# Kernel optimization log

Hardware: AMD Instinct MI355X
Metric: run time of the kernel (lower is better)

Reference implementation:

```python
import jax, jax.numpy as jnp
import numpy as np

L, BATCH, STATE_DIM, HIDDEN, ACTION_DIM = 2048, 32, 256, 1024, 64


def setup_inputs() -> dict:
    key = jax.random.key(0)
    k1, k2, k3, k4 = jax.random.split(key, 4)
    states = jax.random.normal(k1, (L, BATCH, STATE_DIM), dtype=jnp.float32)
    actions = jax.random.normal(k2, (L, BATCH, ACTION_DIM), dtype=jnp.float32)
    # Parameters, matching torch init: A_log = log(0.99), B/C weights ~ N(0, 0.01)
    A_log = jnp.full((HIDDEN,), np.log(0.99), dtype=jnp.float32)
    B_w = 0.01 * jax.random.normal(k3, (HIDDEN, STATE_DIM), dtype=jnp.float32)
    B_b = jnp.zeros((HIDDEN,), dtype=jnp.float32)
    C_w = 0.01 * jax.random.normal(k4, (ACTION_DIM, HIDDEN), dtype=jnp.float32)
    C_b = jnp.zeros((ACTION_DIM,), dtype=jnp.float32)
    log_std = jnp.zeros((ACTION_DIM,), dtype=jnp.float32)
    return {"states": states, "actions": actions, "A_log": A_log,
            "B_w": B_w, "B_b": B_b, "C_w": C_w, "C_b": C_b, "log_std": log_std}


def reference(states, actions, A_log, B_w, B_b, C_w, C_b, log_std):
    # b_t = B(states_t)  -> [L, batch, hidden]
    b = jnp.einsum('lbd,hd->lbh', states, B_w) + B_b
    # log_P[t] = cumsum over seq of broadcast A_log = (t+1) * A_log
    seq = states.shape[0]
    t = jnp.arange(1, seq + 1, dtype=states.dtype)  # [L]
    log_P = t[:, None, None] * A_log[None, None, :]  # [L, 1, hidden]
    P = jnp.exp(log_P)
    # h_t = P_t * cumsum_t(b_t / P_t)  (log-domain linear SSM scan)
    h = P * jnp.cumsum(b / P, axis=0)
    h = jnp.tanh(h)
    mus = jnp.einsum('lbh,ah->lba', h, C_w) + C_b  # [L, batch, action]
    std = jnp.exp(log_std)
    log_pi = (-0.5 * (jnp.log(jnp.asarray(2.0 * np.pi, dtype=mus.dtype)) + 2.0 * log_std)
              - 0.5 * ((actions - mus) / std) ** 2)
    return log_pi.sum(axis=-1)  # [L, batch]; torch squeeze(-1) is a no-op for batch>1
```

## Files before the change

kernel.cpp:

```cpp
#include <hip/hip_runtime.h>
#include <hip/hip_bf16.h>

typedef __attribute__((ext_vector_type(4))) float f32x4;
typedef __attribute__((ext_vector_type(8))) short bf16x8;

#define SDIM 256
#define HID 1024
#define ADIM 64
#define CHUNK 16
#define NCHUNK 128
#define NCH 32768

#define WS8_STB  67108864ull
#define WS8_SCB  100663296ull
#define WS8_BWB  117440512ull
#define WS8_CWB  117964800ull
#define WS8_NEED 118095872ull
#define WS_STB2  134217728ull
#define WS_SBUF2 134217728ull
#define WS_CBUF2 150994944ull
#define WS_BWB2  167772160ull
#define WS_CWB2  168296448ull
#define WS_NEED2 168427520ull

__device__ __forceinline__ unsigned short f2bf(float f) {
  unsigned int u = __float_as_uint(f);
  u += 0x7FFF + ((u >> 16) & 1);
  return (unsigned short)(u >> 16);
}
__device__ __forceinline__ float bf2f(unsigned short h) {
  return __uint_as_float(((unsigned int)h) << 16);
}
__device__ __forceinline__ float fast_exp2(float x) {
  float r;
  asm("v_exp_f32 %0, %1" : "=v"(r) : "v"(x));
  return r;
}
__device__ __forceinline__ float fast_rcp(float x) {
  float r;
  asm("v_rcp_f32 %0, %1" : "=v"(r) : "v"(x));
  return r;
}
#define LOG2E 1.4426950408889634f

#define GLDS16(gp, lp)                                                        \
  __builtin_amdgcn_global_load_lds(                                           \
      (const __attribute__((address_space(1))) unsigned int*)(gp),            \
      (__attribute__((address_space(3))) unsigned int*)(lp), 16, 0, 0)

#define CVT_SN 16777216
#define CVT_BN 262144
#define CVT_CN 65536
__global__ __launch_bounds__(256) void k_cvt(
    const float* __restrict__ s, const float* __restrict__ bw,
    const float* __restrict__ cw, unsigned short* __restrict__ sb,
    unsigned short* __restrict__ bwb, unsigned short* __restrict__ cwb,
    int perm) {
  long long f = ((long long)blockIdx.x * 256 + threadIdx.x) * 8;
  const float* src;
  unsigned short* dst;
  long long idx, didx;
  if (f < CVT_SN) {
    src = s; dst = sb; idx = f;
    if (perm) {
      long long m = f >> 8, col = f & 255;
      didx = ((m & 31) * 2048 + (m >> 5)) * 256 + col;
    } else didx = f;
  } else if (f < CVT_SN + CVT_BN) {
    src = bw; dst = bwb; idx = f - CVT_SN; didx = idx;
  } else {
    src = cw; dst = cwb; idx = f - CVT_SN - CVT_BN; didx = idx;
  }
  float4 a = *reinterpret_cast<const float4*>(src + idx);
  float4 b = *reinterpret_cast<const float4*>(src + idx + 4);
  ushort4 lo, hi;
  lo.x = f2bf(a.x); lo.y = f2bf(a.y); lo.z = f2bf(a.z); lo.w = f2bf(a.w);
  hi.x = f2bf(b.x); hi.y = f2bf(b.y); hi.z = f2bf(b.z); hi.w = f2bf(b.w);
  *reinterpret_cast<ushort4*>(dst + didx) = lo;
  *reinterpret_cast<ushort4*>(dst + didx + 4) = hi;
}

__device__ __forceinline__ void g1_compute(
    const char* bA, const char* bB, f32x4 (&acc)[4][4],
    int wm, int wn, int l15, int g) {
  bf16x8 af[4][2], bfv[4][2];
#pragma unroll
  for (int kk = 0; kk < 2; ++kk) {
    int slotsw = ((kk * 4 + g) ^ (l15 & 7)) * 16;
#pragma unroll
    for (int f = 0; f < 4; ++f) {
      af[f][kk] = *reinterpret_cast<const bf16x8*>(bA + (wm + f * 16 + l15) * 128 + slotsw);
      bfv[f][kk] = *reinterpret_cast<const bf16x8*>(bB + (wn + f * 16 + l15) * 128 + slotsw);
    }
  }
#pragma unroll
  for (int kk = 0; kk < 2; ++kk)
#pragma unroll
    for (int i = 0; i < 4; ++i)
#pragma unroll
      for (int j = 0; j < 4; ++j)
        acc[i][j] = __builtin_amdgcn_mfma_f32_16x16x32_bf16(
            bfv[j][kk], af[i][kk], acc[i][j], 0, 0, 0);
}

#define STAGE1(tile, buf)                                                     \
  {                                                                           \
    const int k0b_ = (tile) * 128;                                            \
    char* dA_ = lds + (buf) * 32768;                                          \
    char* dB_ = lds + 16384 + (buf) * 32768;                                  \
    _Pragma("unroll")                                                         \
    for (int p = 0; p < 4; ++p) {                                             \
      int chunk = wave * 4 + p;                                               \
      GLDS16((const char*)sb + ((size_t)(m0 + chunk * 8 + srow) * SDIM) * 2 + \
                 k0b_ + swslot * 16,                                          \
             dA_ + chunk * 1024);                                             \
      GLDS16((const char*)bwb + ((size_t)(n0 + chunk * 8 + srow) * SDIM) * 2 +\
                 k0b_ + swslot * 16,                                          \
             dB_ + chunk * 1024);                                             \
    }                                                                         \
  }

#define G1_PIPELINE()                                                         \
  STAGE1(0, 0);                                                               \
  for (int t = 0; t < 3; ++t) {                                               \
    const int cur = t & 1;                                                    \
    STAGE1(t + 1, cur ^ 1);                                                   \
    asm volatile("s_waitcnt vmcnt(8)" ::: "memory");                          \
    __builtin_amdgcn_s_barrier();                                             \
    __builtin_amdgcn_sched_barrier(0);                                        \
    g1_compute(lds + cur * 32768, lds + 16384 + cur * 32768, acc, wm, wn,     \
               l15, g);                                                       \
    __builtin_amdgcn_s_barrier();                                             \
    __builtin_amdgcn_sched_barrier(0);                                        \
  }                                                                           \
  asm volatile("s_waitcnt vmcnt(0)" ::: "memory");                            \
  __builtin_amdgcn_s_barrier();                                               \
  __builtin_amdgcn_sched_barrier(0);                                          \
  g1_compute(lds + 32768, lds + 16384 + 32768, acc, wm, wn, l15, g);          \
  __builtin_amdgcn_s_barrier();                                               \
  __builtin_amdgcn_sched_barrier(0);

__global__ __launch_bounds__(256) void k_gemm1p_f(
    const unsigned short* __restrict__ sb, const unsigned short* __restrict__ bwb,
    const float* __restrict__ Bb, const float* __restrict__ A_log,
    unsigned char* __restrict__ bout8, float* __restrict__ Sb) {
  __shared__ char lds[65536];
  const int tid = threadIdx.x;
  const int wave = tid >> 6, lane = tid & 63;
  const int l15 = lane & 15, g = lane >> 4;
  const int bx = blockIdx.x;
  const int swzb = (bx & 7) * 512 + (bx >> 3);
  const int mt = swzb >> 3, nt = swzb & 7;
  const int m0 = mt * 128, n0 = nt * 128;
  const int bb2 = mt >> 4;
  const int c0t = (mt & 15) * 8;
  const int wm = (wave >> 1) * 64, wn = (wave & 1) * 64;
  const int srow = lane >> 3;
  const int swslot = (lane & 7) ^ srow;

  f32x4 acc[4][4];
#pragma unroll
  for (int i = 0; i < 4; i++)
#pragma unroll
    for (int j = 0; j < 4; j++) acc[i][j] = (f32x4){0.f, 0.f, 0.f, 0.f};

  G1_PIPELINE();

  char* wb = lds + wave * 9216;
#pragma unroll
  for (int j = 0; j < 4; ++j) {
    float4 bb = *reinterpret_cast<const float4*>(Bb + n0 + wn + j * 16 + g * 4);
#pragma unroll
    for (int i = 0; i < 4; ++i) {
      ushort4 w;
      w.x = f2bf(acc[i][j][0] + bb.x);
      w.y = f2bf(acc[i][j][1] + bb.y);
      w.z = f2bf(acc[i][j][2] + bb.z);
      w.w = f2bf(acc[i][j][3] + bb.w);
      *reinterpret_cast<ushort4*>(wb + (i * 16 + l15) * 144 + j * 32 + g * 8) = w;
    }
  }
  const int h8 = lane & 7;
  const int lr = lane >> 3;
#pragma unroll
  for (int tt = 0; tt < 8; ++tt) {
    int ml = lr + tt * 8;
    int4 v = *reinterpret_cast<const int4*>(wb + ml * 144 + h8 * 16);
    unsigned int u[4] = {(unsigned)v.x, (unsigned)v.y, (unsigned)v.z,
                         (unsigned)v.w};
    float f[8];
#pragma unroll
    for (int e = 0; e < 8; ++e) {
      unsigned int bits = (e & 1) ? (u[e >> 1] & 0xFFFF0000u) : (u[e >> 1] << 16);
      f[e] = __uint_as_float(bits);
    }
    int d0 = __builtin_amdgcn_cvt_pk_fp8_f32(f[0], f[1], 0, 0);
    d0 = __builtin_amdgcn_cvt_pk_fp8_f32(f[2], f[3], d0, 1);
    int d1 = __builtin_amdgcn_cvt_pk_fp8_f32(f[4], f[5], 0, 0);
    d1 = __builtin_amdgcn_cvt_pk_fp8_f32(f[6], f[7], d1, 1);
    int2 o = {d0, d1};
    *reinterpret_cast<int2*>(bout8 + (size_t)(m0 + wm + ml) * HID + n0 + wn +
                             h8 * 8) = o;
  }
  {
    const int c = lr >> 1, half = lr & 1;
    float a1v[8], a8v[8];
    {
      float4 a0 = *reinterpret_cast<const float4*>(A_log + n0 + wn + h8 * 8);
      float4 a1_ = *reinterpret_cast<const float4*>(A_log + n0 + wn + h8 * 8 + 4);
      float al8[8] = {a0.x, a0.y, a0.z, a0.w, a1_.x, a1_.y, a1_.z, a1_.w};
#pragma unroll
      for (int e = 0; e < 8; ++e) {
        a1v[e] = fast_exp2(al8[e] * LOG2E);
        a8v[e] = fast_exp2(al8[e] * (8.0f * LOG2E));
      }
    }
    float s8[8] = {0.f, 0.f, 0.f, 0.f, 0.f, 0.f, 0.f, 0.f};
#pragma unroll
    for (int j = 0; j < 8; ++j) {
      int ml = c * 16 + half * 8 + j;
      int4 v = *reinterpret_cast<const int4*>(wb + ml * 144 + h8 * 16);
      unsigned int u[4] = {(unsigned)v.x, (unsigned)v.y, (unsigned)v.z,
                           (unsigned)v.w};
#pragma unroll
      for (int e = 0; e < 8; ++e) {
        unsigned int bits = (e & 1) ? (u[e >> 1] & 0xFFFF0000u) : (u[e >> 1] << 16);
        s8[e] = fmaf(a1v[e], s8[e], __uint_as_float(bits));
      }
    }
    const float hsel = half ? 1.0f : 0.0f;
#pragma unroll
    for (int e = 0; e < 8; ++e) {
      float scale = hsel + (1.0f - hsel) * a8v[e];
      s8[e] *= scale;
      s8[e] += __shfl_xor(s8[e], 8);
    }
    if (half == 0) {
      int cg = c0t + (wm >> 4) + c;
      float4 o0 = {s8[0], s8[1], s8[2], s8[3]};
      float4 o1 = {s8[4], s8[5], s8[6], s8[7]};
      float* sp = Sb + (size_t)cg * NCH + bb2 * 1024 + n0 + wn + h8 * 8;
      *reinterpret_cast<float4*>(sp) = o0;
      *reinterpret_cast<float4*>(sp + 4) = o1;
    }
  }
}

__global__ __launch_bounds__(256) void k_gemm1p_7(
    const unsigned short* __restrict__ sb, const unsigned short* __restrict__ bwb,
    const float* __restrict__ Bb, unsigned short* __restrict__ bout) {
  __shared__ char lds[65536];
  const int tid = threadIdx.x;
  const int wave = tid >> 6, lane = tid & 63;
  const int l15 = lane & 15, g = lane >> 4;
  const int bx = blockIdx.x;
  const int swzb = (bx & 7) * 512 + (bx >> 3);
  const int m0 = (swzb >> 3) * 128, n0 = (swzb & 7) * 128;
  const int wm = (wave >> 1) * 64, wn = (wave & 1) * 64;
  const int srow = lane >> 3;
  const int swslot = (lane & 7) ^ srow;

  f32x4 acc[4][4];
#pragma unroll
  for (int i = 0; i < 4; i++)
#pragma unroll
    for (int j = 0; j < 4; j++) acc[i][j] = (f32x4){0.f, 0.f, 0.f, 0.f};

  G1_PIPELINE();

  char* wb = lds + wave * 9216;
#pragma unroll
  for (int j = 0; j < 4; ++j) {
    float4 bb = *reinterpret_cast<const float4*>(Bb + n0 + wn + j * 16 + g * 4);
#pragma unroll
    for (int i = 0; i < 4; ++i) {
      ushort4 w;
      w.x = f2bf(acc[i][j][0] + bb.x);
      w.y = f2bf(acc[i][j][1] + bb.y);
      w.z = f2bf(acc[i][j][2] + bb.z);
      w.w = f2bf(acc[i][j][3] + bb.w);
      *reinterpret_cast<ushort4*>(wb + (i * 16 + l15) * 144 + j * 32 + g * 8) = w;
    }
  }
#pragma unroll
  for (int tt = 0; tt < 8; ++tt) {
    int ml = (lane >> 3) + tt * 8;
    int4 v = *reinterpret_cast<const int4*>(wb + ml * 144 + (lane & 7) * 16);
    int m = m0 + wm + ml;
    size_t dst = ((size_t)(m & 31) * 2048 + (size_t)(m >> 5)) * HID +
                 n0 + wn + (lane & 7) * 8;
    *reinterpret_cast<int4*>(bout + dst) = v;
  }
}

__global__ __launch_bounds__(256) void k_scan_partial(
    const unsigned short* __restrict__ b2, const float* __restrict__ A_log,
    float* __restrict__ Sbuf) {
  int gid = blockIdx.x * 256 + threadIdx.x;
  int ch = (gid & 4095) * 8;
  int c = gid >> 12;
  int bb = ch >> 10;
  int hh = ch & 1023;
  float4 al0 = *reinterpret_cast<const float4*>(A_log + hh);
  float4 al1 = *reinterpret_cast<const float4*>(A_log + hh + 4);
  float a[8] = {__expf(al0.x), __expf(al0.y), __expf(al0.z), __expf(al0.w),
                __expf(al1.x), __expf(al1.y), __expf(al1.z), __expf(al1.w)};
  const unsigned short* p = b2 + (size_t)bb * 2097152 + (size_t)c * CHUNK * HID + hh;
  float s[8] = {0.f, 0.f, 0.f, 0.f, 0.f, 0.f, 0.f, 0.f};
#pragma unroll 4
  for (int j = 0; j < CHUNK; ++j) {
    int4 v = *reinterpret_cast<const int4*>(p + (size_t)j * HID);
    unsigned int u[4] = {(unsigned)v.x, (unsigned)v.y, (unsigned)v.z, (unsigned)v.w};
#pragma unroll
    for (int e = 0; e < 4; ++e) {
      s[2 * e]     = fmaf(a[2 * e],     s[2 * e],     __uint_as_float(u[e] << 16));
      s[2 * e + 1] = fmaf(a[2 * e + 1], s[2 * e + 1], __uint_as_float(u[e] & 0xFFFF0000u));
    }
  }
  float4 o0 = {s[0], s[1], s[2], s[3]}, o1 = {s[4], s[5], s[6], s[7]};
  *reinterpret_cast<float4*>(Sbuf + (size_t)c * NCH + ch) = o0;
  *reinterpret_cast<float4*>(Sbuf + (size_t)c * NCH + ch + 4) = o1;
}

__global__ __launch_bounds__(256) void k_scan_carry(
    const float* __restrict__ Sbuf, const float* __restrict__ A_log,
    float* __restrict__ Cbuf) {
  int ch = blockIdx.x * 256 + threadIdx.x;
  float aL = __expf(A_log[ch & (HID - 1)] * (float)CHUNK);
  float h = 0.f;
  for (int c = 0; c < NCHUNK; ++c) {
    Cbuf[(size_t)c * NCH + ch] = h;
    h = fmaf(aL, h, Sbuf[(size_t)c * NCH + ch]);
  }
}

__global__ __launch_bounds__(256) void k_scan_carry_ip(
    float* __restrict__ SC, const float* __restrict__ A_log) {
  int ch = blockIdx.x * 256 + threadIdx.x;
  float aL = __expf(A_log[ch & (HID - 1)] * (float)CHUNK);
  float h = 0.f;
  for (int c = 0; c < NCHUNK; ++c) {
    float tmp = SC[(size_t)c * NCH + ch];
    SC[(size_t)c * NCH + ch] = h;
    h = fmaf(aL, h, tmp);
  }
}

template <int FP8>
__global__ __launch_bounds__(256) void k_gemm2f_t(
    const void* __restrict__ b2v, const float* __restrict__ actions,
    const unsigned short* __restrict__ cwb, const float* __restrict__ Cb,
    const float* __restrict__ log_std, const float* __restrict__ A_log,
    const float* __restrict__ Cbuf, float* __restrict__ out) {
  __shared__ char lds[49152];
  const int tid = threadIdx.x;
  const int wave = tid >> 6, lane = tid & 63;
  const int l15 = lane & 15, g = lane >> 4;
  const int bq = blockIdx.x;
  const int bb = bq >> 5;
  const int t0 = (bq & 31) * 64;
  const int c0 = t0 >> 4;
  const int wm = wave * 16;
  const int srow = lane >> 3;
  const int swslot = (lane & 7) ^ srow;
  const int sh = tid & 63;
  const int tq = tid >> 6;

  const size_t elemBase = (size_t)bb * 2097152 + (size_t)(t0 + tq * 16) * HID;
  const unsigned char* srcB8 = (const unsigned char*)b2v + elemBase;
  const unsigned short* srcB16 = (const unsigned short*)b2v + elemBase;
  const float* cbBase = Cbuf + (size_t)(c0 + tq) * NCH + bb * 1024;

  f32x4 acc[4];
#pragma unroll
  for (int j = 0; j < 4; j++) acc[j] = (f32x4){0.f, 0.f, 0.f, 0.f};

  unsigned short va[16];
  float a_cur, h_cur, a_nxt = 0.f, h_nxt = 0.f;
  {
#pragma unroll
    for (int p = 0; p < 2; ++p) {
      int chunk = wave * 2 + p;
      GLDS16((const char*)cwb + ((size_t)(chunk * 8 + srow)) * 2048 +
                 swslot * 16,
             lds + 8192 + chunk * 1024);
    }
    a_cur = A_log[sh];
    h_cur = cbBase[sh];
#pragma unroll
    for (int j = 0; j < 16; ++j)
      va[j] = FP8 ? (unsigned short)srcB8[(size_t)j * HID + sh]
                  : srcB16[(size_t)j * HID + sh];
  }

#pragma unroll
  for (int kt = 0; kt < 16; ++kt) {
    char* buf = lds + (kt % 3) * 16384;
    {
      float a = fast_exp2(a_cur * LOG2E);
      float hst = h_cur;
#pragma unroll
      for (int j = 0; j < 16; ++j) {
        float bval = FP8 ? __builtin_amdgcn_cvt_f32_fp8((int)va[j], 0)
                         : bf2f(va[j]);
        hst = fmaf(a, hst, bval);
        float e = fast_exp2(hst * (2.0f * LOG2E));
        float tn = fmaf(-2.0f, fast_rcp(e + 1.0f), 1.0f);
        int row = tq * 16 + j;
        *reinterpret_cast<unsigned short*>(
            buf + row * 128 + ((sh * 2) ^ ((row & 7) << 4))) = f2bf(tn);
      }
    }
    if (kt < 15) {
      char* nbuf = lds + ((kt + 1) % 3) * 16384;
#pragma unroll
      for (int p = 0; p < 2; ++p) {
        int chunk = wave * 2 + p;
        GLDS16((const char*)cwb + ((size_t)(chunk * 8 + srow)) * 2048 +
                   (kt + 1) * 128 + swslot * 16,
               nbuf + 8192 + chunk * 1024);
      }
      const int hg2 = (kt + 1) * 64 + sh;
      a_nxt = A_log[hg2];
      h_nxt = cbBase[hg2];
#pragma unroll
      for (int j = 0; j < 16; ++j)
        va[j] = FP8 ? (unsigned short)srcB8[(size_t)j * HID + hg2]
                    : srcB16[(size_t)j * HID + hg2];
    }
    __builtin_amdgcn_sched_barrier(0);
    asm volatile("s_waitcnt vmcnt(20)" ::: "memory");
    asm volatile("s_waitcnt lgkmcnt(0)" ::: "memory");
    __builtin_amdgcn_s_barrier();
    __builtin_amdgcn_sched_barrier(0);
    bf16x8 af[2], bfv[4][2];
#pragma unroll
    for (int kk = 0; kk < 2; ++kk) {
      int slotsw = ((kk * 4 + g) ^ (l15 & 7)) * 16;
      af[kk] = *reinterpret_cast<const bf16x8*>(buf + (wm + l15) * 128 + slotsw);
#pragma unroll
      for (int f = 0; f < 4; ++f)
        bfv[f][kk] = *reinterpret_cast<const bf16x8*>(
            buf + 8192 + (f * 16 + l15) * 128 + slotsw);
    }
#pragma unroll
    for (int kk = 0; kk < 2; ++kk)
#pragma unroll
      for (int j = 0; j < 4; ++j)
        acc[j] = __builtin_amdgcn_mfma_f32_16x16x32_bf16(
            af[kk], bfv[j][kk], acc[j], 0, 0, 0);
    a_cur = a_nxt;
    h_cur = h_nxt;
  }
  float istd[4], cb[4];
#pragma unroll
  for (int j = 0; j < 4; ++j) {
    int n = j * 16 + l15;
    istd[j] = __expf(-log_std[n]);
    cb[j] = Cb[n];
  }
  float sls = 0.f;
  for (int n = 0; n < ADIM; ++n) sls += log_std[n];
  const float cterm = -32.0f * 1.8378770664093453f - sls;
  const int rb = wm + g * 4;
#pragma unroll
  for (int r = 0; r < 4; ++r) {
    int rl = rb + r;
    int mo = (t0 + rl) * 32 + bb;
    float ss = 0.f;
#pragma unroll
    for (int j = 0; j < 4; ++j) {
      int n = j * 16 + l15;
      float mu = acc[j][r] + cb[j];
      float d = (actions[(size_t)mo * ADIM + n] - mu) * istd[j];
      ss = fmaf(d, d, ss);
    }
    ss += __shfl_xor(ss, 1);
    ss += __shfl_xor(ss, 2);
    ss += __shfl_xor(ss, 4);
    ss += __shfl_xor(ss, 8);
    if (l15 == 0) out[mo] = cterm - 0.5f * ss;
  }
}

extern "C" void kernel_launch(void* const* d_in, const int* in_sizes, int n_in,
                              void* d_out, int out_size, void* d_ws, size_t ws_size,
                              hipStream_t stream) {
  const float* states  = (const float*)d_in[0];
  const float* actions = (const float*)d_in[1];
  const float* A_log   = (const float*)d_in[2];
  const float* B_w     = (const float*)d_in[3];
  const float* B_b     = (const float*)d_in[4];
  const float* C_w     = (const float*)d_in[5];
  const float* C_b     = (const float*)d_in[6];
  const float* log_std = (const float*)d_in[7];
  float* out = (float*)d_out;
  char* ws = (char*)d_ws;

  if (ws_size >= WS8_NEED) {
    unsigned char* bbuf8 = (unsigned char*)ws;
    unsigned short* stb = (unsigned short*)(ws + WS8_STB);
    float* SC = (float*)(ws + WS8_SCB);
    unsigned short* bwb = (unsigned short*)(ws + WS8_BWB);
    unsigned short* cwb = (unsigned short*)(ws + WS8_CWB);
    k_cvt<<<8352, 256, 0, stream>>>(states, B_w, C_w, stb, bwb, cwb, 1);
    k_gemm1p_f<<<4096, 256, 0, stream>>>(stb, bwb, B_b, A_log, bbuf8, SC);
    k_scan_carry_ip<<<128, 256, 0, stream>>>(SC, A_log);
    k_gemm2f_t<1><<<1024, 256, 0, stream>>>(bbuf8, actions, cwb, C_b, log_std,
                                            A_log, SC, out);
  } else {
    unsigned short* bbuf = (unsigned short*)ws;
    unsigned short* stb = (unsigned short*)(ws + WS_STB2);
    float* Sbuf = (float*)(ws + WS_SBUF2);
    float* Cbuf = (float*)(ws + WS_CBUF2);
    unsigned short* bwb = (unsigned short*)(ws + WS_BWB2);
    unsigned short* cwb = (unsigned short*)(ws + WS_CWB2);
    k_cvt<<<8352, 256, 0, stream>>>(states, B_w, C_w, stb, bwb, cwb, 0);
    k_gemm1p_7<<<4096, 256, 0, stream>>>(stb, bwb, B_b, bbuf);
    k_scan_partial<<<2048, 256, 0, stream>>>(bbuf, A_log, Sbuf);
    k_scan_carry<<<128, 256, 0, stream>>>(Sbuf, A_log, Cbuf);
    k_gemm2f_t<0><<<1024, 256, 0, stream>>>(bbuf, actions, cwb, C_b, log_std,
                                            A_log, Cbuf, out);
  }
}
```

Measured before the change: 116.2 us.

## Fuse fp32 states-to-bf16 conversion and permutation into the first GEMM's A loads

The first GEMM now reads fp32 states directly from global memory, applying the batch/time permutation in its addressing, converting to bf16 with packed cvt instructions, and writing into swizzled LDS. The separate conversion pass now only handles the small weight matrices. This removes a full write-and-reread of the 64 MB bf16 states copy. The cost is more global traffic per GEMM tile (fp32 A instead of bf16) and register-staged loads in place of direct global-to-LDS copies, which may weaken the pipeline overlap. The fast path's workspace condition also changes to the larger threshold WS_NEED2.

```diff
diff --git a/kernel.cpp b/kernel.cpp
--- a/kernel.cpp
+++ b/kernel.cpp
@@ -11,11 +11,10 @@
 #define NCHUNK 128
 #define NCH 32768
 
-#define WS8_STB  67108864ull
-#define WS8_SCB  100663296ull
-#define WS8_BWB  117440512ull
-#define WS8_CWB  117964800ull
-#define WS8_NEED 118095872ull
+#define WS8_SCB  67108864ull
+#define WS8_BWB  83886080ull
+#define WS8_CWB  84410368ull
+#define WS8_NEED 84541440ull
 #define WS_STB2  134217728ull
 #define WS_SBUF2 134217728ull
 #define WS_CBUF2 150994944ull
@@ -41,6 +40,11 @@
   asm("v_rcp_f32 %0, %1" : "=v"(r) : "v"(x));
   return r;
 }
+__device__ __forceinline__ unsigned int cvt_pk_bf16(float lo, float hi) {
+  unsigned int r;
+  asm("v_cvt_pk_bf16_f32 %0, %1, %2" : "=v"(r) : "v"(lo), "v"(hi));
+  return r;
+}
 #define LOG2E 1.4426950408889634f
 
 #define GLDS16(gp, lp)                                                        \
@@ -48,36 +52,45 @@
       (const __attribute__((address_space(1))) unsigned int*)(gp),            \
       (__attribute__((address_space(3))) unsigned int*)(lp), 16, 0, 0)
 
-#define CVT_SN 16777216
-#define CVT_BN 262144
-#define CVT_CN 65536
-__global__ __launch_bounds__(256) void k_cvt(
-    const float* __restrict__ s, const float* __restrict__ bw,
-    const float* __restrict__ cw, unsigned short* __restrict__ sb,
-    unsigned short* __restrict__ bwb, unsigned short* __restrict__ cwb,
-    int perm) {
+#define CVTW_BN 262144
+__global__ __launch_bounds__(256) void k_cvt_w(
+    const float* __restrict__ bw, const float* __restrict__ cw,
+    unsigned short* __restrict__ bwb, unsigned short* __restrict__ cwb) {
   long long f = ((long long)blockIdx.x * 256 + threadIdx.x) * 8;
   const float* src;
   unsigned short* dst;
-  long long idx, didx;
-  if (f < CVT_SN) {
-    src = s; dst = sb; idx = f;
-    if (perm) {
-      long long m = f >> 8, col = f & 255;
-      didx = ((m & 31) * 2048 + (m >> 5)) * 256 + col;
-    } else didx = f;
-  } else if (f < CVT_SN + CVT_BN) {
-    src = bw; dst = bwb; idx = f - CVT_SN; didx = idx;
-  } else {
-    src = cw; dst = cwb; idx = f - CVT_SN - CVT_BN; didx = idx;
-  }
+  long long idx;
+  if (f < CVTW_BN) { src = bw; dst = bwb; idx = f; }
+  else { src = cw; dst = cwb; idx = f - CVTW_BN; }
   float4 a = *reinterpret_cast<const float4*>(src + idx);
   float4 b = *reinterpret_cast<const float4*>(src + idx + 4);
   ushort4 lo, hi;
   lo.x = f2bf(a.x); lo.y = f2bf(a.y); lo.z = f2bf(a.z); lo.w = f2bf(a.w);
   hi.x = f2bf(b.x); hi.y = f2bf(b.y); hi.z = f2bf(b.z); hi.w = f2bf(b.w);
-  *reinterpret_cast<ushort4*>(dst + didx) = lo;
-  *reinterpret_cast<ushort4*>(dst + didx + 4) = hi;
+  *reinterpret_cast<ushort4*>(dst + idx) = lo;
+  *reinterpret_cast<ushort4*>(dst + idx + 4) = hi;
+}
+
+#define CVT_SN 16777216
+#define CVT_BN 262144
+__global__ __launch_bounds__(256) void k_cvt(
+    const float* __restrict__ s, const float* __restrict__ bw,
+    const float* __restrict__ cw, unsigned short* __restrict__ sb,
+    unsigned short* __restrict__ bwb, unsigned short* __restrict__ cwb) {
+  long long f = ((long long)blockIdx.x * 256 + threadIdx.x) * 8;
+  const float* src;
+  unsigned short* dst;
+  long long idx;
+  if (f < CVT_SN) { src = s; dst = sb; idx = f; }
+  else if (f < CVT_SN + CVT_BN) { src = bw; dst = bwb; idx = f - CVT_SN; }
+  else { src = cw; dst = cwb; idx = f - CVT_SN - CVT_BN; }
+  float4 a = *reinterpret_cast<const float4*>(src + idx);
+  float4 b = *reinterpret_cast<const float4*>(src + idx + 4);
+  ushort4 lo, hi;
+  lo.x = f2bf(a.x); lo.y = f2bf(a.y); lo.z = f2bf(a.z); lo.w = f2bf(a.w);
+  hi.x = f2bf(b.x); hi.y = f2bf(b.y); hi.z = f2bf(b.z); hi.w = f2bf(b.w);
+  *reinterpret_cast<ushort4*>(dst + idx) = lo;
+  *reinterpret_cast<ushort4*>(dst + idx + 4) = hi;
 }
 
 __device__ __forceinline__ void g1_compute(
@@ -101,6 +114,175 @@
       for (int j = 0; j < 4; ++j)
         acc[i][j] = __builtin_amdgcn_mfma_f32_16x16x32_bf16(
             bfv[j][kk], af[i][kk], acc[i][j], 0, 0, 0);
+}
+
+__global__ __launch_bounds__(256) void k_gemm1p_f(
+    const float* __restrict__ states, const unsigned short* __restrict__ bwb,
+    const float* __restrict__ Bb, const float* __restrict__ A_log,
+    unsigned char* __restrict__ bout8, float* __restrict__ Sb) {
+  __shared__ char lds[65536];
+  const int tid = threadIdx.x;
+  const int wave = tid >> 6, lane = tid & 63;
+  const int l15 = lane & 15, g = lane >> 4;
+  const int bx = blockIdx.x;
+  const int swzb = (bx & 7) * 512 + (bx >> 3);
+  const int mt = swzb >> 3, nt = swzb & 7;
+  const int m0 = mt * 128, n0 = nt * 128;
+  const int bb2 = mt >> 4;
+  const int c0t = (mt & 15) * 8;
+  const int wm = (wave >> 1) * 64, wn = (wave & 1) * 64;
+  const int srow = lane >> 3;
+  const int swslot = (lane & 7) ^ srow;
+  const int t15 = tid & 15;
+  const int rbase8 = tid >> 4;
+  const size_t aBase =
+      ((size_t)(((mt & 15) * 128 + rbase8) * 32 + bb2)) * 256 + t15 * 4;
+
+#define A_LOAD(tile, av)                                                      \
+  _Pragma("unroll")                                                           \
+  for (int i = 0; i < 8; ++i)                                                 \
+    av[i] = *reinterpret_cast<const float4*>(states + aBase +                 \
+                                             (size_t)i * 131072 + (tile) * 64);
+
+#define A_CVT_WRITE(buf, av)                                                  \
+  {                                                                           \
+    char* dA_ = lds + (buf) * 32768;                                          \
+    _Pragma("unroll")                                                         \
+    for (int i = 0; i < 8; ++i) {                                             \
+      int row_ = i * 16 + rbase8;                                             \
+      unsigned int r0_ = cvt_pk_bf16(av[i].x, av[i].y);                       \
+      unsigned int r1_ = cvt_pk_bf16(av[i].z, av[i].w);                       \
+      int off_ = row_ * 128 + (((t15 >> 1) ^ (row_ & 7)) << 4) + (t15 & 1) * 8;\
+      uint2 o_ = {r0_, r1_};                                                  \
+      *reinterpret_cast<uint2*>(dA_ + off_) = o_;                             \
+    }                                                                         \
+  }
+
+#define B_GLDS(tile, buf)                                                     \
+  {                                                                           \
+    char* dB_ = lds + (buf) * 32768 + 16384;                                  \
+    const int k0b_ = (tile) * 128;                                            \
+    _Pragma("unroll")                                                         \
+    for (int p = 0; p < 4; ++p) {                                             \
+      int chunk = wave * 4 + p;                                               \
+      GLDS16((const char*)bwb + ((size_t)(n0 + chunk * 8 + srow) * SDIM) * 2 +\
+                 k0b_ + swslot * 16,                                          \
+             dB_ + chunk * 1024);                                             \
+    }                                                                         \
+  }
+
+  f32x4 acc[4][4];
+#pragma unroll
+  for (int i = 0; i < 4; i++)
+#pragma unroll
+    for (int j = 0; j < 4; j++) acc[i][j] = (f32x4){0.f, 0.f, 0.f, 0.f};
+
+  float4 av[8];
+  A_LOAD(0, av);
+  B_GLDS(0, 0);
+  A_CVT_WRITE(0, av);
+  for (int t = 0; t < 3; ++t) {
+    const int cur = t & 1;
+    A_LOAD(t + 1, av);
+    B_GLDS(t + 1, cur ^ 1);
+    asm volatile("s_waitcnt vmcnt(12)" ::: "memory");
+    asm volatile("s_waitcnt lgkmcnt(0)" ::: "memory");
+    __builtin_amdgcn_s_barrier();
+    __builtin_amdgcn_sched_barrier(0);
+    g1_compute(lds + cur * 32768, lds + cur * 32768 + 16384, acc, wm, wn, l15, g);
+    __builtin_amdgcn_s_barrier();
+    __builtin_amdgcn_sched_barrier(0);
+    A_CVT_WRITE(cur ^ 1, av);
+  }
+  asm volatile("s_waitcnt vmcnt(0)" ::: "memory");
+  asm volatile("s_waitcnt lgkmcnt(0)" ::: "memory");
+  __builtin_amdgcn_s_barrier();
+  __builtin_amdgcn_sched_barrier(0);
+  g1_compute(lds + 32768, lds + 32768 + 16384, acc, wm, wn, l15, g);
+  __builtin_amdgcn_s_barrier();
+  __builtin_amdgcn_sched_barrier(0);
+
+  char* wb = lds + wave * 9216;
+#pragma unroll
+  for (int j = 0; j < 4; ++j) {
+    float4 bb = *reinterpret_cast<const float4*>(Bb + n0 + wn + j * 16 + g * 4);
+#pragma unroll
+    for (int i = 0; i < 4; ++i) {
+      ushort4 w;
+      w.x = f2bf(acc[i][j][0] + bb.x);
+      w.y = f2bf(acc[i][j][1] + bb.y);
+      w.z = f2bf(acc[i][j][2] + bb.z);
+      w.w = f2bf(acc[i][j][3] + bb.w);
+      *reinterpret_cast<ushort4*>(wb + (i * 16 + l15) * 144 + j * 32 + g * 8) = w;
+    }
+  }
+  const int h8 = lane & 7;
+  const int lr = lane >> 3;
+#pragma unroll
+  for (int tt = 0; tt < 8; ++tt) {
+    int ml = lr + tt * 8;
+    int4 v = *reinterpret_cast<const int4*>(wb + ml * 144 + h8 * 16);
+    unsigned int u[4] = {(unsigned)v.x, (unsigned)v.y, (unsigned)v.z,
+                         (unsigned)v.w};
+    float f[8];
+#pragma unroll
+    for (int e = 0; e < 8; ++e) {
+      unsigned int bits = (e & 1) ? (u[e >> 1] & 0xFFFF0000u) : (u[e >> 1] << 16);
+      f[e] = __uint_as_float(bits);
+    }
+    int d0 = __builtin_amdgcn_cvt_pk_fp8_f32(f[0], f[1], 0, 0);
+    d0 = __builtin_amdgcn_cvt_pk_fp8_f32(f[2], f[3], d0, 1);
+    int d1 = __builtin_amdgcn_cvt_pk_fp8_f32(f[4], f[5], 0, 0);
+    d1 = __builtin_amdgcn_cvt_pk_fp8_f32(f[6], f[7], d1, 1);
+    int2 o = {d0, d1};
+    *reinterpret_cast<int2*>(bout8 + (size_t)(m0 + wm + ml) * HID + n0 + wn +
+                             h8 * 8) = o;
+  }
+  {
+    const int c = lr >> 1, half = lr & 1;
+    float a1v[8], a8v[8];
+    {
+      float4 a0 = *reinterpret_cast<const float4*>(A_log + n0 + wn + h8 * 8);
+      float4 a1_ = *reinterpret_cast<const float4*>(A_log + n0 + wn + h8 * 8 + 4);
+      float al8[8] = {a0.x, a0.y, a0.z, a0.w, a1_.x, a1_.y, a1_.z, a1_.w};
+#pragma unroll
+      for (int e = 0; e < 8; ++e) {
+        a1v[e] = fast_exp2(al8[e] * LOG2E);
+        a8v[e] = fast_exp2(al8[e] * (8.0f * LOG2E));
+      }
+    }
+    float s8[8] = {0.f, 0.f, 0.f, 0.f, 0.f, 0.f, 0.f, 0.f};
+#pragma unroll
+    for (int j = 0; j < 8; ++j) {
+      int ml = c * 16 + half * 8 + j;
+      int4 v = *reinterpret_cast<const int4*>(wb + ml * 144 + h8 * 16);
+      unsigned int u[4] = {(unsigned)v.x, (unsigned)v.y, (unsigned)v.z,
+                           (unsigned)v.w};
+#pragma unroll
+      for (int e = 0; e < 8; ++e) {
+        unsigned int bits = (e & 1) ? (u[e >> 1] & 0xFFFF0000u) : (u[e >> 1] << 16);
+        s8[e] = fmaf(a1v[e], s8[e], __uint_as_float(bits));
+      }
+    }
+    const float hsel = half ? 1.0f : 0.0f;
+#pragma unroll
+    for (int e = 0; e < 8; ++e) {
+      float scale = hsel + (1.0f - hsel) * a8v[e];
+      s8[e] *= scale;
+      s8[e] += __shfl_xor(s8[e], 8);
+    }
+    if (half == 0) {
+      int cg = c0t + (wm >> 4) + c;
+      float4 o0 = {s8[0], s8[1], s8[2], s8[3]};
+      float4 o1 = {s8[4], s8[5], s8[6], s8[7]};
+      float* sp = Sb + (size_t)cg * NCH + bb2 * 1024 + n0 + wn + h8 * 8;
+      *reinterpret_cast<float4*>(sp) = o0;
+      *reinterpret_cast<float4*>(sp + 4) = o1;
+    }
+  }
+#undef A_LOAD
+#undef A_CVT_WRITE
+#undef B_GLDS
 }
 
 #define STAGE1(tile, buf)                                                     \
@@ -120,132 +302,6 @@
     }                                                                         \
   }
 
-#define G1_PIPELINE()                                                         \
-  STAGE1(0, 0);                                                               \
-  for (int t = 0; t < 3; ++t) {                                               \
-    const int cur = t & 1;                                                    \
-    STAGE1(t + 1, cur ^ 1);                                                   \
-    asm volatile("s_waitcnt vmcnt(8)" ::: "memory");                          \
-    __builtin_amdgcn_s_barrier();                                             \
-    __builtin_amdgcn_sched_barrier(0);                                        \
-    g1_compute(lds + cur * 32768, lds + 16384 + cur * 32768, acc, wm, wn,     \
-               l15, g);                                                       \
-    __builtin_amdgcn_s_barrier();                                             \
-    __builtin_amdgcn_sched_barrier(0);                                        \
-  }                                                                           \
-  asm volatile("s_waitcnt vmcnt(0)" ::: "memory");                            \
-  __builtin_amdgcn_s_barrier();                                               \
-  __builtin_amdgcn_sched_barrier(0);                                          \
-  g1_compute(lds + 32768, lds + 16384 + 32768, acc, wm, wn, l15, g);          \
-  __builtin_amdgcn_s_barrier();                                               \
-  __builtin_amdgcn_sched_barrier(0);
-
-__global__ __launch_bounds__(256) void k_gemm1p_f(
-    const unsigned short* __restrict__ sb, const unsigned short* __restrict__ bwb,
-    const float* __restrict__ Bb, const float* __restrict__ A_log,
-    unsigned char* __restrict__ bout8, float* __restrict__ Sb) {
-  __shared__ char lds[65536];
-  const int tid = threadIdx.x;
-  const int wave = tid >> 6, lane = tid & 63;
-  const int l15 = lane & 15, g = lane >> 4;
-  const int bx = blockIdx.x;
-  const int swzb = (bx & 7) * 512 + (bx >> 3);
-  const int mt = swzb >> 3, nt = swzb & 7;
-  const int m0 = mt * 128, n0 = nt * 128;
-  const int bb2 = mt >> 4;
-  const int c0t = (mt & 15) * 8;
-  const int wm = (wave >> 1) * 64, wn = (wave & 1) * 64;
-  const int srow = lane >> 3;
-  const int swslot = (lane & 7) ^ srow;
-
-  f32x4 acc[4][4];
-#pragma unroll
-  for (int i = 0; i < 4; i++)
-#pragma unroll
-    for (int j = 0; j < 4; j++) acc[i][j] = (f32x4){0.f, 0.f, 0.f, 0.f};
-
-  G1_PIPELINE();
-
-  char* wb = lds + wave * 9216;
-#pragma unroll
-  for (int j = 0; j < 4; ++j) {
-    float4 bb = *reinterpret_cast<const float4*>(Bb + n0 + wn + j * 16 + g * 4);
-#pragma unroll
-    for (int i = 0; i < 4; ++i) {
-      ushort4 w;
-      w.x = f2bf(acc[i][j][0] + bb.x);
-      w.y = f2bf(acc[i][j][1] + bb.y);
-      w.z = f2bf(acc[i][j][2] + bb.z);
-      w.w = f2bf(acc[i][j][3] + bb.w);
-      *reinterpret_cast<ushort4*>(wb + (i * 16 + l15) * 144 + j * 32 + g * 8) = w;
-    }
-  }
-  const int h8 = lane & 7;
-  const int lr = lane >> 3;
-#pragma unroll
-  for (int tt = 0; tt < 8; ++tt) {
-    int ml = lr + tt * 8;
-    int4 v = *reinterpret_cast<const int4*>(wb + ml * 144 + h8 * 16);
-    unsigned int u[4] = {(unsigned)v.x, (unsigned)v.y, (unsigned)v.z,
-                         (unsigned)v.w};
-    float f[8];
-#pragma unroll
-    for (int e = 0; e < 8; ++e) {
-      unsigned int bits = (e & 1) ? (u[e >> 1] & 0xFFFF0000u) : (u[e >> 1] << 16);
-      f[e] = __uint_as_float(bits);
-    }
-    int d0 = __builtin_amdgcn_cvt_pk_fp8_f32(f[0], f[1], 0, 0);
-    d0 = __builtin_amdgcn_cvt_pk_fp8_f32(f[2], f[3], d0, 1);
-    int d1 = __builtin_amdgcn_cvt_pk_fp8_f32(f[4], f[5], 0, 0);
-    d1 = __builtin_amdgcn_cvt_pk_fp8_f32(f[6], f[7], d1, 1);
-    int2 o = {d0, d1};
-    *reinterpret_cast<int2*>(bout8 + (size_t)(m0 + wm + ml) * HID + n0 + wn +
-                             h8 * 8) = o;
-  }
-  {
-    const int c = lr >> 1, half = lr & 1;
-    float a1v[8], a8v[8];
-    {
-      float4 a0 = *reinterpret_cast<const float4*>(A_log + n0 + wn + h8 * 8);
-      float4 a1_ = *reinterpret_cast<const float4*>(A_log + n0 + wn + h8 * 8 + 4);
-      float al8[8] = {a0.x, a0.y, a0.z, a0.w, a1_.x, a1_.y, a1_.z, a1_.w};
-#pragma unroll
-      for (int e = 0; e < 8; ++e) {
-        a1v[e] = fast_exp2(al8[e] * LOG2E);
-        a8v[e] = fast_exp2(al8[e] * (8.0f * LOG2E));
-      }
-    }
-    float s8[8] = {0.f, 0.f, 0.f, 0.f, 0.f, 0.f, 0.f, 0.f};
-#pragma unroll
-    for (int j = 0; j < 8; ++j) {
-      int ml = c * 16 + half * 8 + j;
-      int4 v = *reinterpret_cast<const int4*>(wb + ml * 144 + h8 * 16);
-      unsigned int u[4] = {(unsigned)v.x, (unsigned)v.y, (unsigned)v.z,
-                           (unsigned)v.w};
-#pragma unroll
-      for (int e = 0; e < 8; ++e) {
-        unsigned int bits = (e & 1) ? (u[e >> 1] & 0xFFFF0000u) : (u[e >> 1] << 16);
-        s8[e] = fmaf(a1v[e], s8[e], __uint_as_float(bits));
-      }
-    }
-    const float hsel = half ? 1.0f : 0.0f;
-#pragma unroll
-    for (int e = 0; e < 8; ++e) {
-      float scale = hsel + (1.0f - hsel) * a8v[e];
-      s8[e] *= scale;
-      s8[e] += __shfl_xor(s8[e], 8);
-    }
-    if (half == 0) {
-      int cg = c0t + (wm >> 4) + c;
-      float4 o0 = {s8[0], s8[1], s8[2], s8[3]};
-      float4 o1 = {s8[4], s8[5], s8[6], s8[7]};
-      float* sp = Sb + (size_t)cg * NCH + bb2 * 1024 + n0 + wn + h8 * 8;
-      *reinterpret_cast<float4*>(sp) = o0;
-      *reinterpret_cast<float4*>(sp + 4) = o1;
-    }
-  }
-}
-
 __global__ __launch_bounds__(256) void k_gemm1p_7(
     const unsigned short* __restrict__ sb, const unsigned short* __restrict__ bwb,
     const float* __restrict__ Bb, unsigned short* __restrict__ bout) {
@@ -266,7 +322,23 @@
 #pragma unroll
     for (int j = 0; j < 4; j++) acc[i][j] = (f32x4){0.f, 0.f, 0.f, 0.f};
 
-  G1_PIPELINE();
+  STAGE1(0, 0);
+  for (int t = 0; t < 3; ++t) {
+    const int cur = t & 1;
+    STAGE1(t + 1, cur ^ 1);
+    asm volatile("s_waitcnt vmcnt(8)" ::: "memory");
+    __builtin_amdgcn_s_barrier();
+    __builtin_amdgcn_sched_barrier(0);
+    g1_compute(lds + cur * 32768, lds + 16384 + cur * 32768, acc, wm, wn, l15, g);
+    __builtin_amdgcn_s_barrier();
+    __builtin_amdgcn_sched_barrier(0);
+  }
+  asm volatile("s_waitcnt vmcnt(0)" ::: "memory");
+  __builtin_amdgcn_s_barrier();
+  __builtin_amdgcn_sched_barrier(0);
+  g1_compute(lds + 32768, lds + 16384 + 32768, acc, wm, wn, l15, g);
+  __builtin_amdgcn_s_barrier();
+  __builtin_amdgcn_sched_barrier(0);
 
   char* wb = lds + wave * 9216;
 #pragma unroll
@@ -497,14 +569,13 @@
   float* out = (float*)d_out;
   char* ws = (char*)d_ws;
 
-  if (ws_size >= WS8_NEED) {
+  if (ws_size >= WS_NEED2) {
     unsigned char* bbuf8 = (unsigned char*)ws;
-    unsigned short* stb = (unsigned short*)(ws + WS8_STB);
     float* SC = (float*)(ws + WS8_SCB);
     unsigned short* bwb = (unsigned short*)(ws + WS8_BWB);
     unsigned short* cwb = (unsigned short*)(ws + WS8_CWB);
-    k_cvt<<<8352, 256, 0, stream>>>(states, B_w, C_w, stb, bwb, cwb, 1);
-    k_gemm1p_f<<<4096, 256, 0, stream>>>(stb, bwb, B_b, A_log, bbuf8, SC);
+    k_cvt_w<<<160, 256, 0, stream>>>(B_w, C_w, bwb, cwb);
+    k_gemm1p_f<<<4096, 256, 0, stream>>>(states, bwb, B_b, A_log, bbuf8, SC);
     k_scan_carry_ip<<<128, 256, 0, stream>>>(SC, A_log);
     k_gemm2f_t<1><<<1024, 256, 0, stream>>>(bbuf8, actions, cwb, C_b, log_std,
                                             A_log, SC, out);
@@ -515,7 +586,7 @@
     float* Cbuf = (float*)(ws + WS_CBUF2);
     unsigned short* bwb = (unsigned short*)(ws + WS_BWB2);
     unsigned short* cwb = (unsigned short*)(ws + WS_CWB2);
-    k_cvt<<<8352, 256, 0, stream>>>(states, B_w, C_w, stb, bwb, cwb, 0);
+    k_cvt<<<8352, 256, 0, stream>>>(states, B_w, C_w, stb, bwb, cwb);
     k_gemm1p_7<<<4096, 256, 0, stream>>>(stb, bwb, B_b, bbuf);
     k_scan_partial<<<2048, 256, 0, stream>>>(bbuf, A_log, Sbuf);
     k_scan_carry<<<128, 256, 0, stream>>>(Sbuf, A_log, Cbuf);
```

Result: no change. 116.7 us (+0.4%).
